# Performance work log

Measured on AMD Instinct MI355X. Metric: run time of the kernel, lower is better.

Reference implementation:

```python
import jax, jax.numpy as jnp
import numpy as np

NUM_PROPOSALS = 200000
NUM_OBJECTS = 128
N_CLS = 256
POS_THR = 0.4
NEG_THR = 0.1
REG_FACTOR = 10.0


def _make_boxes(key, n, img=1000.0, max_wh=200.0):
    k1, k2 = jax.random.split(key)
    xy = jax.random.uniform(k1, (n, 2), jnp.float32) * (img - max_wh)
    wh = jax.random.uniform(k2, (n, 2), jnp.float32) * (max_wh - 1.0) + 1.0
    return jnp.concatenate([xy, xy + wh], axis=-1)  # valid xyxy boxes


def setup_inputs() -> dict:
    key = jax.random.key(0)
    k1, k2, k3 = jax.random.split(key, 3)
    return {
        "objectness_score": jax.random.normal(k1, (NUM_PROPOSALS,), jnp.float32),
        "proposals": _make_boxes(k2, NUM_PROPOSALS),
        "gt_bounding_box": _make_boxes(k3, NUM_OBJECTS)[None],  # (1, N, 4)
    }


def _box_iou(b1, b2):
    # b1: (N,4), b2: (M,4) in xyxy -> (N, M)
    a1 = (b1[:, 2] - b1[:, 0]) * (b1[:, 3] - b1[:, 1])
    a2 = (b2[:, 2] - b2[:, 0]) * (b2[:, 3] - b2[:, 1])
    lt = jnp.maximum(b1[:, None, :2], b2[None, :, :2])
    rb = jnp.minimum(b1[:, None, 2:], b2[None, :, 2:])
    wh = jnp.clip(rb - lt, 0.0)
    inter = wh[..., 0] * wh[..., 1]
    return inter / (a1[:, None] + a2[None, :] - inter)


def _rpn_loss(objectness_score, proposals, gt_bounding_box):
    gt = gt_bounding_box[0]                      # (N, 4)
    iou = _box_iou(gt, proposals)                # (N, M)
    N, M = iou.shape
    flat = iou.reshape(-1)                       # (N*M,)

    # top-N best (gt, proposal) pairs, indices only (non-differentiable path)
    _, best_idx = jax.lax.top_k(flat, N)

    key = jax.random.key(42)
    k1, k2, k3 = jax.random.split(key, 3)
    neg_inf = jnp.float32(-jnp.inf)

    # random-priority sampling == randperm + truncate over candidate multiset
    pos_prio = jnp.where(flat > POS_THR, jax.random.uniform(k1, (N * M,)), neg_inf)
    best_prio = jax.random.uniform(k2, (N,))
    cand_prio = jnp.concatenate([best_prio, pos_prio])
    cand_idx = jnp.concatenate([best_idx, jnp.arange(N * M)])

    num_pos = N_CLS // 2   # always filled: best_idx contributes N=128 candidates
    num_neg = N_CLS - num_pos

    sel_p, loc = jax.lax.top_k(cand_prio, num_pos)
    pos_flat = cand_idx[loc]
    pos_valid = jnp.isfinite(sel_p)
    pos_rows = pos_flat // M
    pos_cols = pos_flat % M

    neg_prio = jnp.where(flat < NEG_THR, jax.random.uniform(k3, (N * M,)), neg_inf)
    sel_n, neg_flat = jax.lax.top_k(neg_prio, num_neg)
    neg_valid = jnp.isfinite(sel_n)
    neg_cols = neg_flat % M

    # classification: BCE-with-logits, mean over valid samples
    logits = jnp.concatenate([objectness_score[pos_cols], objectness_score[neg_cols]])
    labels = jnp.concatenate([jnp.ones((num_pos,), jnp.float32), jnp.zeros((num_neg,), jnp.float32)])
    w = jnp.concatenate([pos_valid, neg_valid]).astype(jnp.float32)
    bce = jnp.maximum(logits, 0.0) - logits * labels + jnp.log1p(jnp.exp(-jnp.abs(logits)))
    cls_loss = jnp.sum(bce * w) / jnp.maximum(jnp.sum(w), 1.0)

    d = proposals[pos_cols] - gt[pos_rows]       # (num_pos, 4)
    ad = jnp.abs(d)
    sl1 = jnp.where(ad < 1.0, 0.5 * d * d, ad - 0.5)
    wp = pos_valid.astype(jnp.float32)[:, None]
    reg_loss = jnp.sum(sl1 * wp) / jnp.maximum(jnp.sum(wp) * 4.0, 1.0)

    return cls_loss + REG_FACTOR * reg_loss


def reference(objectness_score, proposals, gt_bounding_box):
    return _rpn_loss(objectness_score, proposals, gt_bounding_box)
```

## Files before the change

### kernel.cpp

```cpp
#include <hip/hip_runtime.h>
#include <stdint.h>

#pragma clang fp contract(off)

typedef unsigned long long u64;
typedef uint32_t u32;

#define M_PROP 200000u
#define N_GT   128u
#define NM     25600000u

#define BCUT 8355840u
#define CCUT 8387584u
#define IB_POS 0x3ECCCCCDu

#define SHARDS 16u
#define SHARD_CAP 4096u
#define ACAP_SHARD 65536u
#define TOPA_CAP 8192u
#define COMP_CAP 8192u
#define ALIST 512u

#define NBX 782u
#define NT_A (NBX * 2u)
#define NT_ALL (NBX * 6u)
#define PERSIST 2048u

#define CSLOT(i) counters[(u32)(i) * 64u]

__device__ inline u32 rotl32(u32 x, u32 r) { return __builtin_rotateleft32(x, r); }

__device__ inline u32 lane_prefix(u64 mask) {
  return __builtin_amdgcn_mbcnt_hi((u32)(mask >> 32),
                                   __builtin_amdgcn_mbcnt_lo((u32)mask, 0u));
}

__host__ __device__ inline void tf2x32(u32 k0, u32 k1, u32 x0, u32 x1,
                                       u32& o0, u32& o1) {
  u32 ks0 = k0, ks1 = k1, ks2 = k0 ^ k1 ^ 0x1BD11BDAu;
  x0 += ks0; x1 += ks1;
#ifdef __HIP_DEVICE_COMPILE__
#define TF_R(r) { x0 += x1; x1 = rotl32(x1, r); x1 ^= x0; }
#else
#define TF_R(r) { x0 += x1; x1 = (x1 << r) | (x1 >> (32 - r)); x1 ^= x0; }
#endif
  TF_R(13) TF_R(15) TF_R(26) TF_R(6)
  x0 += ks1; x1 += ks2 + 1u;
  TF_R(17) TF_R(29) TF_R(16) TF_R(24)
  x0 += ks2; x1 += ks0 + 2u;
  TF_R(13) TF_R(15) TF_R(26) TF_R(6)
  x0 += ks0; x1 += ks1 + 3u;
  TF_R(17) TF_R(29) TF_R(16) TF_R(24)
  x0 += ks1; x1 += ks2 + 4u;
  TF_R(13) TF_R(15) TF_R(26) TF_R(6)
  x0 += ks2; x1 += ks0 + 5u;
#undef TF_R
  o0 = x0; o1 = x1;
}

__device__ inline u32 jax_bits32(u32 ka, u32 kb, u32 idx) {
  u32 a, b; tf2x32(ka, kb, 0u, idx, a, b);
  return a ^ b;
}

static void jax_split3(u32& k1a, u32& k1b, u32& k2a, u32& k2b,
                       u32& k3a, u32& k3b) {
  const u32 K0 = 0u, K1 = 42u;
  tf2x32(K0, K1, 0u, 0u, k1a, k1b);
  tf2x32(K0, K1, 0u, 1u, k2a, k2b);
  tf2x32(K0, K1, 0u, 2u, k3a, k3b);
}

__device__ inline u32 wave_append_slot(u32* ctr, bool pred, bool& any) {
  u64 mask = __ballot(pred);
  if (mask == 0ull) { any = false; return 0u; }
  any = true;
  u32 prefix = lane_prefix(mask);
  int leader = __ffsll(mask) - 1;
  u32 base = 0u;
  if ((int)(threadIdx.x & 63u) == leader)
    base = atomicAdd(ctr, (u32)__popcll(mask));
  base = __shfl(base, leader, 64);
  return base + prefix;
}

__device__ inline u32 iouBin(u32 bits) {
  u32 b = (bits - 0x3E800000u) >> 14;
  return b > 1023u ? 1023u : b;
}

__global__ __launch_bounds__(256, 8) void rpn_collect(
    const float4* __restrict__ props, const float4* __restrict__ gt,
    u64* __restrict__ bufA, u64* __restrict__ bufB, u64* __restrict__ bufC,
    u32* __restrict__ counters, u32* __restrict__ gHistA,
    u32 k1a, u32 k1b, u32 k3a, u32 k3b) {
  __shared__ float4 gtS[64];
  __shared__ float gtAreaS[64];
  __shared__ u32 hA[1024];
  __shared__ u32 listA[4][ALIST];
  const u32 tid = threadIdx.x;
  const u32 lane = tid & 63u;
  const u32 wid = tid >> 6;
  for (u32 i = tid; i < 1024u; i += 256u) hA[i] = 0u;

  for (u32 t = blockIdx.x; t < NT_ALL; t += PERSIST) {
    __syncthreads();
    const u32 shard = t & (SHARDS - 1u);
    if (t < NT_A) {
      const u32 bx = t >> 1;
      const u32 gbase = (t & 1u) * 64u;
      for (u32 j = tid; j < 64u; j += 256u) {
        float4 gb = gt[gbase + j];
        gtS[j] = gb;
        gtAreaS[j] = (gb.z - gb.x) * (gb.w - gb.y);
      }
      __syncthreads();
      u32* cntB_g = &CSLOT(16u + shard);
      u32* cntA_g = &CSLOT(32u + shard);
      u64* myBufB = bufB + (size_t)shard * SHARD_CAP;
      u64* myBufA = bufA + (size_t)shard * ACAP_SHARD;

      u32 p = bx * 256u + tid;
      bool active = p < M_PROP;
      float4 pb = make_float4(0.f, 0.f, 0.f, 0.f);
      if (active) pb = props[p];
      float pa = (pb.z - pb.x) * (pb.w - pb.y);
      u32 cntA = 0u;

#define PROCESS_A()                                                          \
      {                                                                      \
        for (u32 i = lane; i < cntA; i += 64u) {                             \
          u32 aidx = listA[wid][i];                                          \
          u32 row = aidx / M_PROP;                                           \
          u32 col = aidx - row * M_PROP;                                     \
          float4 pbx = props[col];                                           \
          float4 gbx = gtS[row - gbase];                                     \
          float gax = gtAreaS[row - gbase];                                  \
          float pax = (pbx.z - pbx.x) * (pbx.w - pbx.y);                     \
          float wxx = fminf(gbx.z, pbx.z) - fmaxf(gbx.x, pbx.x);             \
          float wyy = fminf(gbx.w, pbx.w) - fmaxf(gbx.y, pbx.y);             \
          wxx = fmaxf(wxx, 0.0f); wyy = fmaxf(wyy, 0.0f);                    \
          float interx = wxx * wyy;                                          \
          float ioux = interx / (gax + pax - interx);                        \
          u32 ib = __float_as_uint(ioux);                                    \
          bool isA = ioux > 0.25f;                                           \
          if (isA) atomicAdd(&hA[iouBin(ib)], 1u);                           \
          bool anyk;                                                         \
          u32 sk = wave_append_slot(cntA_g, isA, anyk);                      \
          if (isA && sk < ACAP_SHARD)                                        \
            myBufA[sk] = ((u64)ib << 25) | (u64)(0x1FFFFFFu - aidx);         \
          u32 m1 = jax_bits32(k1a, k1b, aidx) >> 9;                          \
          bool keep = isA && (ib > IB_POS) && (m1 >= BCUT);                  \
          bool anyb;                                                         \
          u32 sb2 = wave_append_slot(cntB_g, keep, anyb);                    \
          if (keep && sb2 < SHARD_CAP)                                       \
            myBufB[sb2] = ((u64)m1 << 25) | (u64)(0x1FFFFFFu - (aidx + 128u)); \
        }                                                                    \
        cntA = 0u;                                                           \
      }

      for (u32 gg = 0u; gg < 64u; gg += 4u) {
        bool aa[4];
#pragma unroll
        for (u32 r = 0u; r < 4u; ++r) {
          float4 gb = gtS[gg + r];
          float ga = gtAreaS[gg + r];
          float wx = fminf(gb.z, pb.z) - fmaxf(gb.x, pb.x);
          float wy = fminf(gb.w, pb.w) - fmaxf(gb.y, pb.y);
          wx = fmaxf(wx, 0.0f); wy = fmaxf(wy, 0.0f);
          float inter = wx * wy;
          float uni = ga + pa - inter;
          aa[r] = active && (inter > 0.2499f * uni);
        }
#pragma unroll
        for (u32 r = 0u; r < 4u; ++r) {
          u64 ma = __ballot(aa[r]);
          if (ma) {
            u32 pfx = lane_prefix(ma);
            if (aa[r]) listA[wid][cntA + pfx] = (gbase + gg + r) * M_PROP + p;
            cntA += (u32)__popcll(ma);
          }
        }
        if (cntA > ALIST - 256u) PROCESS_A();
      }
      PROCESS_A();
#undef PROCESS_A
    } else {
      const u32 ct = t - NT_A;
      const u32 bx = ct >> 2;
      const u32 gbase = (ct & 3u) * 32u;
      for (u32 j = tid; j < 32u; j += 256u) {
        float4 gb = gt[gbase + j];
        gtS[j] = gb;
        gtAreaS[j] = (gb.z - gb.x) * (gb.w - gb.y);
      }
      __syncthreads();
      u32* cntC_g = &CSLOT(shard);
      u64* myBufC = bufC + (size_t)shard * SHARD_CAP;

      u32 p = bx * 256u + tid;
      bool active = p < M_PROP;

      for (u32 gg = 0u; gg < 32u; gg += 8u) {
        const u32 ibase = (gbase + gg) * M_PROP + p;
#define TFCH(R) u32 m3_##R; { u32 a_, b_; \
        tf2x32(k3a, k3b, 0u, ibase + (R) * M_PROP, a_, b_); \
        m3_##R = (a_ ^ b_) >> 9; }
        TFCH(0) TFCH(1) TFCH(2) TFCH(3) TFCH(4) TFCH(5) TFCH(6) TFCH(7)
#undef TFCH
        bool pre0 = m3_0 >= CCUT, pre1 = m3_1 >= CCUT;
        bool pre2 = m3_2 >= CCUT, pre3 = m3_3 >= CCUT;
        bool pre4 = m3_4 >= CCUT, pre5 = m3_5 >= CCUT;
        bool pre6 = m3_6 >= CCUT, pre7 = m3_7 >= CCUT;
        bool anyp = pre0 | pre1 | pre2 | pre3 | pre4 | pre5 | pre6 | pre7;
        if (__ballot(anyp)) {
          float4 pbx = make_float4(0.f, 0.f, 0.f, 0.f);
          if (active) pbx = props[p];
          float pax = (pbx.z - pbx.x) * (pbx.w - pbx.y);
#define CRARE(R)                                                             \
          {                                                                  \
            float4 gb = gtS[gg + (R)];                                       \
            float ga = gtAreaS[gg + (R)];                                    \
            float wx = fminf(gb.z, pbx.z) - fmaxf(gb.x, pbx.x);              \
            float wy = fminf(gb.w, pbx.w) - fmaxf(gb.y, pbx.y);              \
            wx = fmaxf(wx, 0.0f); wy = fmaxf(wy, 0.0f);                      \
            float inter = wx * wy;                                           \
            float iouX = inter / (ga + pax - inter);                         \
            bool cc = active && pre##R && (iouX < 0.1f);                     \
            bool any_;                                                       \
            u32 s = wave_append_slot(cntC_g, cc, any_);                      \
            if (cc && s < SHARD_CAP)                                         \
              myBufC[s] = ((u64)m3_##R << 25) |                              \
                          (u64)(0x1FFFFFFu - (ibase + (R) * M_PROP));        \
          }
          CRARE(0) CRARE(1) CRARE(2) CRARE(3)
          CRARE(4) CRARE(5) CRARE(6) CRARE(7)
#undef CRARE
        }
      }
    }
  }

  __syncthreads();
  for (u32 b = tid; b < 1024u; b += 256u) {
    u32 v = hA[b];
    if (v) atomicAdd(&gHistA[b], v);
  }
}

__global__ __launch_bounds__(256) void rpn_filterA(
    const u64* __restrict__ bufA, const u32* __restrict__ gHistA,
    u32* __restrict__ counters, u64* __restrict__ bufTopA) {
  const u32 tid = threadIdx.x;
  const u32 lane = tid & 63u;
  u32 loc[16]; u32 t = 0u;
  const u32 bbase = lane * 16u;
#pragma unroll
  for (u32 j = 0u; j < 16u; ++j) { loc[j] = gHistA[bbase + j]; t += loc[j]; }
  u32 suf = t;
  for (u32 off = 1u; off < 64u; off <<= 1u) {
    u32 o = __shfl_down(suf, off, 64);
    if (lane + off < 64u) suf += o;
  }
  u32 cum = suf - t;
  u32 cand = 0u; bool found = false;
#pragma unroll
  for (int j = 15; j >= 0; --j) {
    cum += loc[j];
    if (!found && cum >= 128u) { cand = bbase + (u32)j; found = true; }
  }
  for (u32 off = 1u; off < 64u; off <<= 1u) {
    u32 o = __shfl_xor(cand, off, 64);
    cand = o > cand ? o : cand;
  }
  const u32 cut = cand;
  const u32 sh = blockIdx.x & (SHARDS - 1u);
  const u32 chunk = blockIdx.x >> 4;
  u32 n = CSLOT(32u + sh); n = n < ACAP_SHARD ? n : ACAP_SHARD;
  const u64* sb = bufA + (size_t)sh * ACAP_SHARD;
  for (u32 i = chunk * 256u + tid; i < n; i += 16u * 256u) {
    u64 k = sb[i];
    bool keep = iouBin((u32)(k >> 25)) >= cut;
    bool any;
    u32 s = wave_append_slot(&CSLOT(48), keep, any);
    if (keep && s < TOPA_CAP) bufTopA[s] = k;
  }
}

__device__ inline void rank_select(const u64* cand, u32 nc, u64* selKey) {
  const u32 tid = threadIdx.x;
  if (tid < 128u) selKey[tid] = 0ull;
  u64 k[8]; u32 r[8];
#pragma unroll
  for (int j = 0; j < 8; ++j) {
    u32 i = tid + (u32)j * 1024u;
    k[j] = (i < nc) ? cand[i] : 0ull;
    r[j] = 0u;
  }
  __syncthreads();
  for (u32 i = 0u; i < nc; ++i) {
    u64 v = cand[i];
#pragma unroll
    for (int j = 0; j < 8; ++j) r[j] += (v > k[j]) ? 1u : 0u;
  }
#pragma unroll
  for (int j = 0; j < 8; ++j) {
    u32 i = tid + (u32)j * 1024u;
    if (i < nc && r[j] < 128u) selKey[r[j]] = k[j];
  }
  __syncthreads();
}

__device__ inline void rank_select2(const u64* cand, u32 nc, u64* selKey) {
  const u32 tid = threadIdx.x;
  if (tid < 128u) selKey[tid] = 0ull;
  u64 mine = (tid < nc) ? cand[tid] : 0ull;
  __syncthreads();
  u32 r = 0u;
  for (u32 i = 0u; i < nc; ++i) r += (cand[i] > mine) ? 1u : 0u;
  if (tid < nc && r < 128u) selKey[r] = mine;
  __syncthreads();
}

__device__ inline float sl1(float d) {
  float ad = fabsf(d);
  return (ad < 1.0f) ? 0.5f * d * d : ad - 0.5f;
}

__global__ __launch_bounds__(1024) void rpn_finalize(
    const float* __restrict__ obj, const float4* __restrict__ props,
    const float4* __restrict__ gt,
    const u64* __restrict__ bufTopA,
    const u64* __restrict__ bufB, const u64* __restrict__ bufC,
    const u32* __restrict__ counters, float* __restrict__ out,
    u32 k2a, u32 k2b) {
  __shared__ u64 keyBuf[COMP_CAP];
  __shared__ u64 keyBuf2[1024];
  __shared__ u64 selKey[128];
  __shared__ u32 bestIdx[128];
  __shared__ u32 hist64[64];
  __shared__ float pr[16];
  __shared__ u32 s_cnt, s_cnt2, s_cutLo;
  __shared__ float s_reg, s_bcep;

  const u32 tid = threadIdx.x;
  const u32 lane = tid & 63u;
  const u32 wid = tid >> 6u;

  u32 nT = CSLOT(48); nT = nT < TOPA_CAP ? nT : TOPA_CAP;
  for (u32 i = tid; i < nT; i += 1024u) keyBuf[i] = bufTopA[i];
  __syncthreads();
  if (nT <= 1024u) rank_select2(keyBuf, nT, selKey);
  else rank_select(keyBuf, nT, selKey);
  if (tid < 128u) {
    u64 k = selKey[tid];
    bestIdx[tid] = (k == 0ull) ? 0u : (0x1FFFFFFu - (u32)(k & 0x1FFFFFFu));
  }
  __syncthreads();

  if (tid == 0u) { s_cnt = 128u; s_cnt2 = 0u; }
  if (tid < 64u) hist64[tid] = 0u;
  __syncthreads();
  if (tid < 128u) {
    u32 m2 = jax_bits32(k2a, k2b, tid) >> 9;
    keyBuf[tid] = ((u64)m2 << 25) | (u64)(0x1FFFFFFu - tid);
    if (m2 >= BCUT) atomicAdd(&hist64[(m2 - BCUT) >> 9], 1u);
  }
  {
    u32 n = CSLOT(16u + wid); n = n < SHARD_CAP ? n : SHARD_CAP;
    const u64* sb = bufB + (size_t)wid * SHARD_CAP;
    for (u32 i = lane; i < n; i += 64u) {
      u64 k = sb[i];
      bool any;
      u32 s = wave_append_slot(&s_cnt, true, any);
      if (s < COMP_CAP) keyBuf[s] = k;
      atomicAdd(&hist64[((u32)(k >> 25) - BCUT) >> 9], 1u);
    }
  }
  __syncthreads();
  u32 nc = s_cnt < COMP_CAP ? s_cnt : COMP_CAP;
  if (wid == 0u) {
    u32 suf = hist64[lane];
    for (u32 off = 1u; off < 64u; off <<= 1u) {
      u32 o = __shfl_down(suf, off, 64);
      if (lane + off < 64u) suf += o;
    }
    u64 ok = __ballot(suf >= 128u);
    u32 cutLo = 0u;
    if (ok) cutLo = BCUT + ((63u - (u32)__clzll(ok)) << 9);
    if (lane == 0u) s_cutLo = cutLo;
  }
  __syncthreads();
  {
    u64 cutKey = ((u64)s_cutLo) << 25;
    for (u32 i = tid; i < nc; i += 1024u) {
      u64 k = keyBuf[i];
      if (k >= cutKey) {
        u32 s = atomicAdd(&s_cnt2, 1u);
        if (s < 1024u) keyBuf2[s] = k;
      }
    }
  }
  __syncthreads();
  u32 ns = s_cnt2;
  if (ns <= 1024u) rank_select2(keyBuf2, ns, selKey);
  else rank_select(keyBuf, nc, selKey);

  float locReg = 0.0f, locBce = 0.0f;
  if (tid < 128u) {
    u64 k = selKey[tid];
    if (k != 0ull) {
      u32 c = 0x1FFFFFFu - (u32)(k & 0x1FFFFFFu);
      u32 pair = (c < 128u) ? bestIdx[c] : (c - 128u);
      if (pair < NM) {
        u32 row = pair / M_PROP, col = pair % M_PROP;
        float4 prb = props[col];
        float4 gb = gt[row];
        locReg = sl1(prb.x - gb.x) + sl1(prb.y - gb.y) +
                 sl1(prb.z - gb.z) + sl1(prb.w - gb.w);
        float l = obj[col];
        locBce = fmaxf(l, 0.0f) - l + log1pf(expf(-fabsf(l)));
      }
    }
  }
  {
    float v = locReg;
    for (u32 off = 32u; off > 0u; off >>= 1u) v += __shfl_xor(v, off, 64);
    if (lane == 0u) pr[wid] = v;
    __syncthreads();
    if (tid == 0u) {
      float s = 0.0f;
#pragma unroll
      for (u32 w = 0u; w < 16u; ++w) s += pr[w];
      s_reg = s;
    }
    __syncthreads();
    v = locBce;
    for (u32 off = 32u; off > 0u; off >>= 1u) v += __shfl_xor(v, off, 64);
    if (lane == 0u) pr[wid] = v;
    __syncthreads();
    if (tid == 0u) {
      float s = 0.0f;
#pragma unroll
      for (u32 w = 0u; w < 16u; ++w) s += pr[w];
      s_bcep = s;
    }
    __syncthreads();
  }

  if (tid == 0u) { s_cnt = 0u; s_cnt2 = 0u; }
  if (tid < 64u) hist64[tid] = 0u;
  __syncthreads();
  {
    u32 n = CSLOT(wid); n = n < SHARD_CAP ? n : SHARD_CAP;
    const u64* sb = bufC + (size_t)wid * SHARD_CAP;
    for (u32 i = lane; i < n; i += 64u) {
      u64 k = sb[i];
      bool any;
      u32 s = wave_append_slot(&s_cnt, true, any);
      if (s < COMP_CAP) keyBuf[s] = k;
      atomicAdd(&hist64[((u32)(k >> 25) - CCUT) >> 4], 1u);
    }
  }
  __syncthreads();
  nc = s_cnt < COMP_CAP ? s_cnt : COMP_CAP;
  if (wid == 0u) {
    u32 suf = hist64[lane];
    for (u32 off = 1u; off < 64u; off <<= 1u) {
      u32 o = __shfl_down(suf, off, 64);
      if (lane + off < 64u) suf += o;
    }
    u64 ok = __ballot(suf >= 128u);
    u32 cutLo = 0u;
    if (ok) cutLo = CCUT + ((63u - (u32)__clzll(ok)) << 4);
    if (lane == 0u) s_cutLo = cutLo;
  }
  __syncthreads();
  {
    u64 cutKey = ((u64)s_cutLo) << 25;
    for (u32 i = tid; i < nc; i += 1024u) {
      u64 k = keyBuf[i];
      if (k >= cutKey) {
        u32 s = atomicAdd(&s_cnt2, 1u);
        if (s < 1024u) keyBuf2[s] = k;
      }
    }
  }
  __syncthreads();
  ns = s_cnt2;
  if (ns <= 1024u) rank_select2(keyBuf2, ns, selKey);
  else rank_select(keyBuf, nc, selKey);

  float locBceN = 0.0f;
  if (tid < 128u) {
    u64 k = selKey[tid];
    if (k != 0ull) {
      u32 idx = 0x1FFFFFFu - (u32)(k & 0x1FFFFFFu);
      u32 col = idx % M_PROP;
      float l = obj[col];
      locBceN = fmaxf(l, 0.0f) + log1pf(expf(-fabsf(l)));
    }
  }
  {
    float v = locBceN;
    for (u32 off = 32u; off > 0u; off >>= 1u) v += __shfl_xor(v, off, 64);
    if (lane == 0u) pr[wid] = v;
    __syncthreads();
    if (tid == 0u) {
      float s = 0.0f;
#pragma unroll
      for (u32 w = 0u; w < 16u; ++w) s += pr[w];
      float cls = (s_bcep + s) / 256.0f;
      float reg = s_reg / 512.0f;
      out[0] = cls + 10.0f * reg;
    }
  }
}

extern "C" void kernel_launch(void* const* d_in, const int* in_sizes, int n_in,
                              void* d_out, int out_size, void* d_ws, size_t ws_size,
                              hipStream_t stream) {
  (void)in_sizes; (void)n_in; (void)out_size; (void)ws_size;
  const float* obj = (const float*)d_in[0];
  const float4* props = (const float4*)d_in[1];
  const float4* gt = (const float4*)d_in[2];
  float* out = (float*)d_out;

  u32 k1a, k1b, k2a, k2b, k3a, k3b;
  jax_split3(k1a, k1b, k2a, k2b, k3a, k3b);

  uint8_t* base = (uint8_t*)d_ws;
  u32* counters = (u32*)base;
  u32* gHistA = (u32*)(base + 16384);
  u64* bufTopA = (u64*)(base + 16384 + 4096);
  u64* bufB = (u64*)(base + 16384 + 4096 + (size_t)TOPA_CAP * 8);
  u64* bufC = bufB + (size_t)SHARDS * SHARD_CAP;
  u64* bufA = bufC + (size_t)SHARDS * SHARD_CAP;

  hipMemsetAsync(d_ws, 0, 16384 + 4096, stream);
  rpn_collect<<<PERSIST, 256, 0, stream>>>(
      props, gt, bufA, bufB, bufC, counters, gHistA, k1a, k1b, k3a, k3b);
  rpn_filterA<<<256, 256, 0, stream>>>(bufA, gHistA, counters, bufTopA);
  rpn_finalize<<<1, 1024, 0, stream>>>(obj, props, gt, bufTopA, bufB, bufC,
                                       counters, out, k2a, k2b);
}
```

Before: 95.64 us.

## Use atomic work-stealing tile queue, schedule C tiles first, hoist threefry keys

The persistent collect kernel now pulls tiles from a global atomic counter instead of a fixed blockIdx stride. The heavy threefry-bound C (negative) tiles are ordered before the A tiles so load balancing is better. Threefry key-schedule constants are hoisted out of the loop, and the eight hash streams are interleaved round by round with a raw-bit threshold compare, which avoids recomputing the key schedule and adds ILP. The counter slot must be reset before each launch, and each tile fetch adds an extra atomic and barrier.

```diff
diff --git a/kernel.cpp b/kernel.cpp
--- a/kernel.cpp
+++ b/kernel.cpp
@@ -12,6 +12,7 @@
 
 #define BCUT 8355840u
 #define CCUT 8387584u
+#define CCUT_RAW 0xFFF80000u
 #define IB_POS 0x3ECCCCCDu
 
 #define SHARDS 16u
@@ -22,7 +23,7 @@
 #define ALIST 512u
 
 #define NBX 782u
-#define NT_A (NBX * 2u)
+#define NT_C (NBX * 4u)
 #define NT_ALL (NBX * 6u)
 #define PERSIST 2048u
 
@@ -98,17 +99,102 @@
   __shared__ float gtAreaS[64];
   __shared__ u32 hA[1024];
   __shared__ u32 listA[4][ALIST];
+  __shared__ u32 s_tile;
   const u32 tid = threadIdx.x;
   const u32 lane = tid & 63u;
   const u32 wid = tid >> 6;
   for (u32 i = tid; i < 1024u; i += 256u) hA[i] = 0u;
 
-  for (u32 t = blockIdx.x; t < NT_ALL; t += PERSIST) {
-    __syncthreads();
+  const u32 ks0 = k3a, ks1 = k3b, ks2 = k3a ^ k3b ^ 0x1BD11BDAu;
+  const u32 i1 = ks2 + 1u, i2 = ks0 + 2u, i3 = ks1 + 3u;
+  const u32 i4 = ks2 + 4u, i5 = ks0 + 5u;
+
+  for (;;) {
+    __syncthreads();
+    if (tid == 0u) s_tile = atomicAdd(&CSLOT(56), 1u);
+    __syncthreads();
+    const u32 t = s_tile;
+    if (t >= NT_ALL) break;
     const u32 shard = t & (SHARDS - 1u);
-    if (t < NT_A) {
-      const u32 bx = t >> 1;
-      const u32 gbase = (t & 1u) * 64u;
+
+    if (t < NT_C) {
+      const u32 bx = t >> 2;
+      const u32 gbase = (t & 3u) * 32u;
+      for (u32 j = tid; j < 32u; j += 256u) {
+        float4 gb = gt[gbase + j];
+        gtS[j] = gb;
+        gtAreaS[j] = (gb.z - gb.x) * (gb.w - gb.y);
+      }
+      __syncthreads();
+      u32* cntC_g = &CSLOT(shard);
+      u64* myBufC = bufC + (size_t)shard * SHARD_CAP;
+
+      u32 p = bx * 256u + tid;
+      bool active = p < M_PROP;
+
+      for (u32 gg = 0u; gg < 32u; gg += 8u) {
+        const u32 ibase = (gbase + gg) * M_PROP + p;
+#define ALL8(OP) OP(0) OP(1) OP(2) OP(3) OP(4) OP(5) OP(6) OP(7)
+#define TFI(i) u32 x0_##i = ks0, x1_##i = (ibase + (i) * M_PROP) + ks1;
+        ALL8(TFI)
+#undef TFI
+#define TFR0(i) x0_##i += x1_##i; x1_##i = rotl32(x1_##i, RT); x1_##i ^= x0_##i;
+#define RND(rot) { const u32 RT = rot; ALL8(TFR0) }
+#define INJ(a, b) { ALL8(TFJ) }
+#define TFJ(i) x0_##i += KA; x1_##i += KB;
+        { const u32 KA = 0u; (void)KA; }
+        RND(13) RND(15) RND(26) RND(6)
+        { const u32 KA = ks1, KB = i1; ALL8(TFJ) }
+        RND(17) RND(29) RND(16) RND(24)
+        { const u32 KA = ks2, KB = i2; ALL8(TFJ) }
+        RND(13) RND(15) RND(26) RND(6)
+        { const u32 KA = ks0, KB = i3; ALL8(TFJ) }
+        RND(17) RND(29) RND(16) RND(24)
+        { const u32 KA = ks1, KB = i4; ALL8(TFJ) }
+        RND(13) RND(15) RND(26) RND(6)
+        { const u32 KA = ks2, KB = i5; ALL8(TFJ) }
+#undef TFJ
+#undef INJ
+#undef RND
+#undef TFR0
+#define TFO(i) const u32 ab_##i = x0_##i ^ x1_##i;
+        ALL8(TFO)
+#undef TFO
+        bool pre0 = ab_0 >= CCUT_RAW, pre1 = ab_1 >= CCUT_RAW;
+        bool pre2 = ab_2 >= CCUT_RAW, pre3 = ab_3 >= CCUT_RAW;
+        bool pre4 = ab_4 >= CCUT_RAW, pre5 = ab_5 >= CCUT_RAW;
+        bool pre6 = ab_6 >= CCUT_RAW, pre7 = ab_7 >= CCUT_RAW;
+        bool anyp = pre0 | pre1 | pre2 | pre3 | pre4 | pre5 | pre6 | pre7;
+        if (__ballot(anyp)) {
+          float4 pbx = make_float4(0.f, 0.f, 0.f, 0.f);
+          if (active) pbx = props[p];
+          float pax = (pbx.z - pbx.x) * (pbx.w - pbx.y);
+#define CRARE(R)                                                             \
+          {                                                                  \
+            float4 gb = gtS[gg + (R)];                                       \
+            float ga = gtAreaS[gg + (R)];                                    \
+            float wx = fminf(gb.z, pbx.z) - fmaxf(gb.x, pbx.x);              \
+            float wy = fminf(gb.w, pbx.w) - fmaxf(gb.y, pbx.y);              \
+            wx = fmaxf(wx, 0.0f); wy = fmaxf(wy, 0.0f);                      \
+            float inter = wx * wy;                                           \
+            float iouX = inter / (ga + pax - inter);                         \
+            bool cc = active && pre##R && (iouX < 0.1f);                     \
+            bool any_;                                                       \
+            u32 s = wave_append_slot(cntC_g, cc, any_);                      \
+            if (cc && s < SHARD_CAP)                                         \
+              myBufC[s] = ((u64)(ab_##R >> 9) << 25) |                       \
+                          (u64)(0x1FFFFFFu - (ibase + (R) * M_PROP));        \
+          }
+          CRARE(0) CRARE(1) CRARE(2) CRARE(3)
+          CRARE(4) CRARE(5) CRARE(6) CRARE(7)
+#undef CRARE
+        }
+#undef ALL8
+      }
+    } else {
+      const u32 u = t - NT_C;
+      const u32 bx = u >> 1;
+      const u32 gbase = (u & 1u) * 64u;
       for (u32 j = tid; j < 64u; j += 256u) {
         float4 gb = gt[gbase + j];
         gtS[j] = gb;
@@ -185,59 +271,6 @@
       }
       PROCESS_A();
 #undef PROCESS_A
-    } else {
-      const u32 ct = t - NT_A;
-      const u32 bx = ct >> 2;
-      const u32 gbase = (ct & 3u) * 32u;
-      for (u32 j = tid; j < 32u; j += 256u) {
-        float4 gb = gt[gbase + j];
-        gtS[j] = gb;
-        gtAreaS[j] = (gb.z - gb.x) * (gb.w - gb.y);
-      }
-      __syncthreads();
-      u32* cntC_g = &CSLOT(shard);
-      u64* myBufC = bufC + (size_t)shard * SHARD_CAP;
-
-      u32 p = bx * 256u + tid;
-      bool active = p < M_PROP;
-
-      for (u32 gg = 0u; gg < 32u; gg += 8u) {
-        const u32 ibase = (gbase + gg) * M_PROP + p;
-#define TFCH(R) u32 m3_##R; { u32 a_, b_; \
-        tf2x32(k3a, k3b, 0u, ibase + (R) * M_PROP, a_, b_); \
-        m3_##R = (a_ ^ b_) >> 9; }
-        TFCH(0) TFCH(1) TFCH(2) TFCH(3) TFCH(4) TFCH(5) TFCH(6) TFCH(7)
-#undef TFCH
-        bool pre0 = m3_0 >= CCUT, pre1 = m3_1 >= CCUT;
-        bool pre2 = m3_2 >= CCUT, pre3 = m3_3 >= CCUT;
-        bool pre4 = m3_4 >= CCUT, pre5 = m3_5 >= CCUT;
-        bool pre6 = m3_6 >= CCUT, pre7 = m3_7 >= CCUT;
-        bool anyp = pre0 | pre1 | pre2 | pre3 | pre4 | pre5 | pre6 | pre7;
-        if (__ballot(anyp)) {
-          float4 pbx = make_float4(0.f, 0.f, 0.f, 0.f);
-          if (active) pbx = props[p];
-          float pax = (pbx.z - pbx.x) * (pbx.w - pbx.y);
-#define CRARE(R)                                                             \
-          {                                                                  \
-            float4 gb = gtS[gg + (R)];                                       \
-            float ga = gtAreaS[gg + (R)];                                    \
-            float wx = fminf(gb.z, pbx.z) - fmaxf(gb.x, pbx.x);              \
-            float wy = fminf(gb.w, pbx.w) - fmaxf(gb.y, pbx.y);              \
-            wx = fmaxf(wx, 0.0f); wy = fmaxf(wy, 0.0f);                      \
-            float inter = wx * wy;                                           \
-            float iouX = inter / (ga + pax - inter);                         \
-            bool cc = active && pre##R && (iouX < 0.1f);                     \
-            bool any_;                                                       \
-            u32 s = wave_append_slot(cntC_g, cc, any_);                      \
-            if (cc && s < SHARD_CAP)                                         \
-              myBufC[s] = ((u64)m3_##R << 25) |                              \
-                          (u64)(0x1FFFFFFu - (ibase + (R) * M_PROP));        \
-          }
-          CRARE(0) CRARE(1) CRARE(2) CRARE(3)
-          CRARE(4) CRARE(5) CRARE(6) CRARE(7)
-#undef CRARE
-        }
-      }
     }
   }
 
```

Measured after the change: 118.6 us. +24.0%, slower.
